# Kernel optimization log

Measured on AMD Instinct MI355X. Metric: run time of the kernel, lower is better.

The kernel has to match this reference:

```python
import jax, jax.numpy as jnp
import numpy as np

E = 256
H_HEADS = 8
HD = E // H_HEADS
NEG = -1e9


def setup_inputs() -> dict:
    key = jax.random.key(0)
    ks = jax.random.split(key, 16)
    B, Q, Hh, Ww = 16, 100, 64, 64
    S = Hh * Ww
    std = 1.0 / np.sqrt(E)
    inp = {
        "query_features": jax.random.normal(ks[0], (B, Q, E), jnp.float32),
        "image_features": jax.random.normal(ks[1], (B, E, Hh, Ww), jnp.float32),
        "mask": jax.random.randint(ks[2], (B, Q, Hh, Ww), 0, 2) > 0,
        "pos_query_embeddings": jax.random.normal(ks[3], (B, Q, E), jnp.float32),
        "pos_image_embeddings": jax.random.normal(ks[4], (B, S, E), jnp.float32),
        "Wq": jax.random.normal(ks[5], (E, E), jnp.float32) * std,
        "bq": jnp.zeros((E,), jnp.float32),
        "Wk": jax.random.normal(ks[6], (E, E), jnp.float32) * std,
        "bk": jnp.zeros((E,), jnp.float32),
        "Wv": jax.random.normal(ks[7], (E, E), jnp.float32) * std,
        "bv": jnp.zeros((E,), jnp.float32),
        "Wo": jax.random.normal(ks[8], (E, E), jnp.float32) * std,
        "bo": jnp.zeros((E,), jnp.float32),
    }
    return inp


def reference(query_features, image_features, mask, pos_query_embeddings,
              pos_image_embeddings, Wq, bq, Wk, bk, Wv, bv, Wo, bo):
    B, _, Hh, Ww = image_features.shape
    Q = query_features.shape[1]
    S = Hh * Ww
    # (B, S, E)
    img = jnp.transpose(image_features.reshape(B, E, S), (0, 2, 1))
    q = (query_features + pos_query_embeddings) @ Wq.T + bq  # (B,Q,E)
    k = (img + pos_image_embeddings) @ Wk.T + bk              # (B,S,E)
    v = img @ Wv.T + bv                                       # (B,S,E)
    q = q.reshape(B, Q, H_HEADS, HD).transpose(0, 2, 1, 3)    # (B,H,Q,D)
    k = k.reshape(B, S, H_HEADS, HD).transpose(0, 2, 1, 3)    # (B,H,S,D)
    v = v.reshape(B, S, H_HEADS, HD).transpose(0, 2, 1, 3)
    scale = 1.0 / jnp.sqrt(jnp.asarray(HD, q.dtype))
    scores = jnp.einsum('bhqd,bhsd->bhqs', q, k) * scale
    amask = mask.reshape(B, 1, Q, S)
    scores = jnp.where(amask, scores, NEG)
    attn = jax.nn.softmax(scores, axis=-1)
    out = jnp.einsum('bhqs,bhsd->bhqd', attn, v)
    out = out.transpose(0, 2, 1, 3).reshape(B, Q, E)
    return out @ Wo.T + bo
```

## Files before the change

### kernel.cpp

```cpp
#include <hip/hip_runtime.h>
#include <math.h>

#define BB 16
#define QQ 100
#define EE 256
#define NH 8
#define HD 32
#define SS 4096
#define QP 128
#define NZ 8
#define SCHUNK (SS / NZ)
#define M0 8.0f

typedef _Float16 half8_t __attribute__((ext_vector_type(8)));
typedef _Float16 half4_t __attribute__((ext_vector_type(4)));
typedef float floatx4 __attribute__((ext_vector_type(4)));

__global__ __launch_bounds__(256) void maskpack_kernel(
    const int* __restrict__ mask, unsigned* __restrict__ mbits)
{
    int gid  = blockIdx.x * 256 + threadIdx.x;
    int lane = gid & 63;
    int F    = gid & ~63;
    int s    = (F & (SS - 1)) + lane;
    int qp   = (F >> 12) & (QP - 1);
    int b    = F >> 19;
    int qc   = min(qp, QQ - 1);
    int v    = mask[((size_t)(b * QQ + qc)) * SS + s];
    unsigned long long bal = __ballot(v != 0);
    int w = (F & (SS - 1)) >> 5;
    if (lane == 0)
        mbits[((size_t)(b * (SS / 32) + w)) * QP + qp] = (unsigned)bal;
    if (lane == 32)
        mbits[((size_t)(b * (SS / 32) + w + 1)) * QP + qp] = (unsigned)(bal >> 32);
}

__global__ __launch_bounds__(256) void wcvt_kernel(
    const float* __restrict__ Wk, const float* __restrict__ Wv,
    _Float16* __restrict__ wk16a, _Float16* __restrict__ wv16a)
{
    int gid = blockIdx.x * 256 + threadIdx.x;
    int m = gid & 8191;
    const float* src = (gid < 8192) ? Wk : Wv;
    _Float16* dst = (gid < 8192) ? wk16a : wv16a;
    int l = m & 63, kk = (m >> 6) & 7, et = m >> 9;
    int e = et * 16 + (l & 15);
    int f0 = kk * 32 + (l >> 4) * 8;
    float4 a0 = *(const float4*)&src[(size_t)e * EE + f0];
    float4 a1 = *(const float4*)&src[(size_t)e * EE + f0 + 4];
    half8_t h;
    h[0]=(_Float16)a0.x; h[1]=(_Float16)a0.y; h[2]=(_Float16)a0.z; h[3]=(_Float16)a0.w;
    h[4]=(_Float16)a1.x; h[5]=(_Float16)a1.y; h[6]=(_Float16)a1.z; h[7]=(_Float16)a1.w;
    *(half8_t*)&dst[(size_t)m * 8] = h;
}

__global__ __launch_bounds__(512, 4) void fused_kv_kernel(
    const float* __restrict__ img,
    const float* __restrict__ pos,
    const _Float16* __restrict__ wk16a, const float* __restrict__ bk,
    const _Float16* __restrict__ wv16a, const float* __restrict__ bv,
    _Float16* __restrict__ kbuf,
    _Float16* __restrict__ vt)
{
    __shared__ _Float16 vstage[256 * 72];

    const int t  = threadIdx.x;
    const int w  = t >> 6, l = t & 63;
    const int gg = l >> 4, li = l & 15;
    const int si = w & 3, eh = w >> 2;

    const int m0  = blockIdx.x * 64;
    const int b   = m0 >> 12;
    const int s0  = m0 & (SS - 1);
    const int ss0 = s0 + si * 16;
    const int e0  = eh * 128;

    const float* imgp = img + (size_t)b * EE * SS + (size_t)(gg * 8) * SS + ss0 + li;
    const float* posp = pos + ((size_t)(b * SS + ss0 + li)) * EE + gg * 8;
    const _Float16* wkp = wk16a + (size_t)eh * 32768 + l * 8;
    const _Float16* wvp = wv16a + (size_t)eh * 32768 + l * 8;

    floatx4 acck[8] = {};
    floatx4 accv[8] = {};

    #pragma unroll 1
    for (int kk = 0; kk < 8; ++kk) {
        const int f0 = kk * 32;

        float iv[8];
        #pragma unroll
        for (int j = 0; j < 8; ++j)
            iv[j] = imgp[(size_t)(f0 + j) * SS];
        float4 p0 = *(const float4*)(posp + f0);
        float4 p1 = *(const float4*)(posp + f0 + 4);

        half8_t av8, ak8;
        av8[0] = (_Float16)iv[0];  ak8[0] = (_Float16)(iv[0] + p0.x);
        av8[1] = (_Float16)iv[1];  ak8[1] = (_Float16)(iv[1] + p0.y);
        av8[2] = (_Float16)iv[2];  ak8[2] = (_Float16)(iv[2] + p0.z);
        av8[3] = (_Float16)iv[3];  ak8[3] = (_Float16)(iv[3] + p0.w);
        av8[4] = (_Float16)iv[4];  ak8[4] = (_Float16)(iv[4] + p1.x);
        av8[5] = (_Float16)iv[5];  ak8[5] = (_Float16)(iv[5] + p1.y);
        av8[6] = (_Float16)iv[6];  ak8[6] = (_Float16)(iv[6] + p1.z);
        av8[7] = (_Float16)iv[7];  ak8[7] = (_Float16)(iv[7] + p1.w);

        #pragma unroll
        for (int n = 0; n < 8; ++n) {
            half8_t wkf = *(const half8_t*)(wkp + (size_t)((n * 8 + kk) << 9));
            half8_t wvf = *(const half8_t*)(wvp + (size_t)((n * 8 + kk) << 9));
            acck[n] = __builtin_amdgcn_mfma_f32_16x16x32_f16(ak8, wkf, acck[n], 0, 0, 0);
            accv[n] = __builtin_amdgcn_mfma_f32_16x16x32_f16(av8, wvf, accv[n], 0, 0, 0);
        }
    }

    #pragma unroll
    for (int n = 0; n < 8; ++n) {
        int e = e0 + n * 16 + li;
        float bj = bk[e];
        int row = b * SS + ss0 + gg * 4;
        #pragma unroll
        for (int r = 0; r < 4; ++r)
            kbuf[(size_t)(row + r) * EE + e] = (_Float16)(acck[n][r] + bj);
    }

    #pragma unroll
    for (int n = 0; n < 8; ++n) {
        int e_loc = e0 + n * 16 + li;
        float bj = bv[e_loc];
        int s_loc = si * 16 + gg * 4;
        half4_t h4;
        #pragma unroll
        for (int r = 0; r < 4; ++r)
            h4[r] = (_Float16)(accv[n][r] + bj);
        *(half4_t*)&vstage[e_loc * 72 + s_loc] = h4;
    }
    __syncthreads();
    #pragma unroll
    for (int c = 0; c < 4; ++c) {
        int row = c * 64 + (t >> 3);
        int so  = (t & 7) * 8;
        half8_t v8 = *(const half8_t*)&vstage[row * 72 + so];
        int hh = row >> 5, dd = row & 31;
        *(half8_t*)(vt + ((size_t)((b * NH + hh) * HD + dd)) * SS + s0 + so) = v8;
    }
}

__global__ __launch_bounds__(256) void proj_kernel(
    const float* __restrict__ x1, const float* __restrict__ x2,
    const float* __restrict__ W, const float* __restrict__ bias,
    float* __restrict__ outf, _Float16* __restrict__ out16,
    float oscale, int has_x2)
{
    const int row0 = blockIdx.x * 8;
    const int t = threadIdx.x;
    __shared__ float xs[8][256];

    #pragma unroll
    for (int p = 0; p < 8; ++p) {
        int idx = t + p * 256;
        int f = idx & 255, j = idx >> 8;
        size_t g = (size_t)(row0 + j) * EE + f;
        float v = x1[g];
        if (has_x2) v += x2[g];
        xs[j][f] = v;
    }
    __syncthreads();

    const int e = t;
    const float* wrow = W + (size_t)e * EE;
    float acc[8];
    const float bv = bias[e];
    #pragma unroll
    for (int j = 0; j < 8; ++j) acc[j] = bv;

    #pragma unroll 4
    for (int f4 = 0; f4 < 64; ++f4) {
        float4 w4 = *(const float4*)(wrow + f4 * 4);
        #pragma unroll
        for (int j = 0; j < 8; ++j) {
            float4 x4 = *(const float4*)&xs[j][f4 * 4];
            acc[j] = fmaf(w4.x, x4.x, acc[j]);
            acc[j] = fmaf(w4.y, x4.y, acc[j]);
            acc[j] = fmaf(w4.z, x4.z, acc[j]);
            acc[j] = fmaf(w4.w, x4.w, acc[j]);
        }
    }
    if (out16) {
        #pragma unroll
        for (int j = 0; j < 8; ++j)
            out16[(size_t)(row0 + j) * EE + e] = (_Float16)(acc[j] * oscale);
    } else {
        #pragma unroll
        for (int j = 0; j < 8; ++j)
            outf[(size_t)(row0 + j) * EE + e] = acc[j];
    }
}

__global__ __launch_bounds__(256) void attn_mfma_kernel(
    const _Float16* __restrict__ q16,
    const _Float16* __restrict__ kbuf,
    const _Float16* __restrict__ vt,
    const unsigned* __restrict__ mbits,
    float* __restrict__ part,
    float* __restrict__ pl)
{
    const int z = blockIdx.x, h = blockIdx.y, b = blockIdx.z;
    const int t = threadIdx.x;
    const int w = t >> 6, l = t & 63;
    const int g = l >> 4, li = l & 15;

    __shared__ _Float16 ks[64 * 40];
    __shared__ _Float16 vs[32 * 72];
    __shared__ _Float16 ps[128 * 72];
    __shared__ unsigned mw[2][QP];

    half8_t qf[2];
    {
        int q0r = min(32 * w + li, QQ - 1);
        int q1r = min(32 * w + 16 + li, QQ - 1);
        qf[0] = *(const half8_t*)(q16 + ((size_t)(b * QQ + q0r)) * EE + h * HD + g * 8);
        qf[1] = *(const half8_t*)(q16 + ((size_t)(b * QQ + q1r)) * EE + h * HD + g * 8);
    }

    float lsum[2][4] = {{0.f}};
    floatx4 accO[2][2] = {};

    for (int it = 0; it < SCHUNK / 64; ++it) {
        const int sblk = z * SCHUNK + it * 64;

        {
            int sl = t >> 2, koff = (t & 3) * 8;
            *(half8_t*)&ks[sl * 40 + koff] =
                *(const half8_t*)(kbuf + ((size_t)(b * SS + sblk + sl)) * EE + h * HD + koff);
            int dl = t >> 3, soff = (t & 7) * 8;
            *(half8_t*)&vs[dl * 72 + soff] =
                *(const half8_t*)(vt + ((size_t)((b * NH + h) * HD + dl)) * SS + sblk + soff);
            mw[t >> 7][t & 127] =
                mbits[((size_t)(b * (SS / 32) + (sblk >> 5) + (t >> 7))) * QP + (t & 127)];
        }
        __syncthreads();

        half8_t kf[4];
        #pragma unroll
        for (int st = 0; st < 4; ++st)
            kf[st] = *(const half8_t*)&ks[(st * 16 + li) * 40 + g * 8];
        floatx4 sc[2][4];
        #pragma unroll
        for (int qt = 0; qt < 2; ++qt)
            #pragma unroll
            for (int st = 0; st < 4; ++st) {
                floatx4 zero = {0.f, 0.f, 0.f, 0.f};
                sc[qt][st] = __builtin_amdgcn_mfma_f32_16x16x32_f16(
                    qf[qt], kf[st], zero, 0, 0, 0);
            }

        #pragma unroll
        for (int qt = 0; qt < 2; ++qt) {
            int qrow0 = 32 * w + qt * 16 + 4 * g;
            unsigned w0r[4], w1r[4];
            #pragma unroll
            for (int r = 0; r < 4; ++r) {
                w0r[r] = mw[0][qrow0 + r];
                w1r[r] = mw[1][qrow0 + r];
            }
            #pragma unroll
            for (int st = 0; st < 4; ++st)
                #pragma unroll
                for (int r = 0; r < 4; ++r) {
                    unsigned word = (st < 2) ? w0r[r] : w1r[r];
                    int keep = (word >> ((st & 1) * 16 + li)) & 1;
                    float pv = keep ? __expf(sc[qt][st][r] - M0) : 0.f;
                    _Float16 ph = (_Float16)pv;
                    lsum[qt][r] += (float)ph;
                    ps[(qrow0 + r) * 72 + st * 16 + li] = ph;
                }
        }

        half8_t vb[2][2];
        #pragma unroll
        for (int dt = 0; dt < 2; ++dt) {
            vb[dt][0] = *(const half8_t*)&vs[(dt * 16 + li) * 72 + g * 8];
            vb[dt][1] = *(const half8_t*)&vs[(dt * 16 + li) * 72 + 32 + g * 8];
        }
        #pragma unroll
        for (int qt = 0; qt < 2; ++qt) {
            half8_t a0 = *(const half8_t*)&ps[(32 * w + qt * 16 + li) * 72 + g * 8];
            half8_t a1 = *(const half8_t*)&ps[(32 * w + qt * 16 + li) * 72 + 32 + g * 8];
            #pragma unroll
            for (int dt = 0; dt < 2; ++dt) {
                accO[qt][dt] = __builtin_amdgcn_mfma_f32_16x16x32_f16(
                    a0, vb[dt][0], accO[qt][dt], 0, 0, 0);
                accO[qt][dt] = __builtin_amdgcn_mfma_f32_16x16x32_f16(
                    a1, vb[dt][1], accO[qt][dt], 0, 0, 0);
            }
        }
        __syncthreads();
    }

    #pragma unroll
    for (int qt = 0; qt < 2; ++qt)
        #pragma unroll
        for (int r = 0; r < 4; ++r) {
            float v = lsum[qt][r];
            v += __shfl_xor(v, 1, 64);
            v += __shfl_xor(v, 2, 64);
            v += __shfl_xor(v, 4, 64);
            v += __shfl_xor(v, 8, 64);
            lsum[qt][r] = v;
        }

    const size_t pbase = (((size_t)z * BB + b) * NH + h) * QP;
    #pragma unroll
    for (int qt = 0; qt < 2; ++qt) {
        int qrow0 = 32 * w + qt * 16 + 4 * g;
        #pragma unroll
        for (int r = 0; r < 4; ++r) {
            int qp = qrow0 + r;
            #pragma unroll
            for (int dt = 0; dt < 2; ++dt)
                part[(pbase + qp) * HD + dt * 16 + li] = accO[qt][dt][r];
            if (li == 0) pl[pbase + qp] = lsum[qt][r];
        }
    }
}

__global__ __launch_bounds__(256) void combine_kernel(
    const float* __restrict__ part, const float* __restrict__ pl,
    float* __restrict__ abuf)
{
    int tid = blockIdx.x * 256 + threadIdx.x;
    int d  = tid & 31;
    int qp = (tid >> 5) & 127;
    int h  = (tid >> 12) & 7;
    int b  = tid >> 15;
    if (qp >= QQ) return;
    float L = 0.f, O = 0.f;
    #pragma unroll
    for (int zz = 0; zz < NZ; ++zz) {
        size_t idx = (((size_t)zz * BB + b) * NH + h) * QP + qp;
        L += pl[idx];
        O += part[idx * HD + d];
    }
    abuf[((size_t)(b * QQ + qp)) * EE + h * HD + d] = O / fmaxf(L, 1e-30f);
}

extern "C" void kernel_launch(void* const* d_in, const int* in_sizes, int n_in,
                              void* d_out, int out_size, void* d_ws, size_t ws_size,
                              hipStream_t stream)
{
    const float* qf   = (const float*)d_in[0];
    const float* img  = (const float*)d_in[1];
    const int*   mask = (const int*)  d_in[2];
    const float* pq   = (const float*)d_in[3];
    const float* pimg = (const float*)d_in[4];
    const float* Wq   = (const float*)d_in[5];
    const float* bq   = (const float*)d_in[6];
    const float* Wk   = (const float*)d_in[7];
    const float* bk   = (const float*)d_in[8];
    const float* Wv   = (const float*)d_in[9];
    const float* bv   = (const float*)d_in[10];
    const float* Wo   = (const float*)d_in[11];
    const float* bo   = (const float*)d_in[12];
    float* out = (float*)d_out;

    const size_t MSE = (size_t)BB * SS * EE;

    _Float16* kbuf = (_Float16*)d_ws;
    _Float16* vtb  = kbuf + MSE;
    _Float16* q16  = vtb + MSE;
    unsigned* mbits = (unsigned*)(q16 + (size_t)BB * QQ * EE);
    float* part = (float*)(mbits + (size_t)BB * (SS / 32) * QP);
    float* pl   = part + (size_t)NZ * BB * NH * QP * HD;
    float* abuf = pl + (size_t)NZ * BB * NH * QP;
    _Float16* wk16a = (_Float16*)(abuf + (size_t)BB * QQ * EE);
    _Float16* wv16a = wk16a + (size_t)EE * EE;

    const float scale = 0.17677669529663687f;

    maskpack_kernel<<<(BB * QP * SS) / 256, 256, 0, stream>>>(mask, mbits);
    wcvt_kernel<<<64, 256, 0, stream>>>(Wk, Wv, wk16a, wv16a);
    proj_kernel<<<BB * QQ / 8, 256, 0, stream>>>(qf, pq, Wq, bq, nullptr, q16, scale, 1);
    fused_kv_kernel<<<BB * SS / 64, 512, 0, stream>>>(img, pimg, wk16a, bk, wv16a, bv, kbuf, vtb);
    attn_mfma_kernel<<<dim3(NZ, NH, BB), 256, 0, stream>>>(q16, kbuf, vtb, mbits, part, pl);
    combine_kernel<<<(BB * NH * QP * HD) / 256, 256, 0, stream>>>(part, pl, abuf);
    proj_kernel<<<BB * QQ / 8, 256, 0, stream>>>(abuf, nullptr, Wo, bo, out, nullptr, 1.f, 0);
}
```

Baseline: 349.2 us.

## Shrink KV projection tile and software-prefetch next input slice

Result: slower. 365.1 us (+4.5%).

```diff
diff --git a/kernel.cpp b/kernel.cpp
--- a/kernel.cpp
+++ b/kernel.cpp
@@ -62,59 +62,79 @@
     _Float16* __restrict__ kbuf,
     _Float16* __restrict__ vt)
 {
-    __shared__ _Float16 vstage[256 * 72];
+    __shared__ _Float16 vstage[256 * 40];
 
     const int t  = threadIdx.x;
     const int w  = t >> 6, l = t & 63;
     const int gg = l >> 4, li = l & 15;
-    const int si = w & 3, eh = w >> 2;
-
-    const int m0  = blockIdx.x * 64;
+    const int si = w & 1, eh = w >> 1;
+
+    const int m0  = blockIdx.x * 32;
     const int b   = m0 >> 12;
     const int s0  = m0 & (SS - 1);
     const int ss0 = s0 + si * 16;
-    const int e0  = eh * 128;
+    const int e0  = eh * 64;
 
     const float* imgp = img + (size_t)b * EE * SS + (size_t)(gg * 8) * SS + ss0 + li;
     const float* posp = pos + ((size_t)(b * SS + ss0 + li)) * EE + gg * 8;
-    const _Float16* wkp = wk16a + (size_t)eh * 32768 + l * 8;
-    const _Float16* wvp = wv16a + (size_t)eh * 32768 + l * 8;
-
-    floatx4 acck[8] = {};
-    floatx4 accv[8] = {};
+    const _Float16* wkp = wk16a + (size_t)eh * 16384 + l * 8;
+    const _Float16* wvp = wv16a + (size_t)eh * 16384 + l * 8;
+
+    floatx4 acck[4] = {};
+    floatx4 accv[4] = {};
+
+    float iva[8], ppa[8];
+    #pragma unroll
+    for (int j = 0; j < 8; ++j) iva[j] = imgp[(size_t)j * SS];
+    {
+        float4 q0 = *(const float4*)posp;
+        float4 q1 = *(const float4*)(posp + 4);
+        ppa[0]=q0.x; ppa[1]=q0.y; ppa[2]=q0.z; ppa[3]=q0.w;
+        ppa[4]=q1.x; ppa[5]=q1.y; ppa[6]=q1.z; ppa[7]=q1.w;
+    }
 
     #pragma unroll 1
     for (int kk = 0; kk < 8; ++kk) {
-        const int f0 = kk * 32;
-
-        float iv[8];
-        #pragma unroll
-        for (int j = 0; j < 8; ++j)
-            iv[j] = imgp[(size_t)(f0 + j) * SS];
-        float4 p0 = *(const float4*)(posp + f0);
-        float4 p1 = *(const float4*)(posp + f0 + 4);
-
         half8_t av8, ak8;
-        av8[0] = (_Float16)iv[0];  ak8[0] = (_Float16)(iv[0] + p0.x);
-        av8[1] = (_Float16)iv[1];  ak8[1] = (_Float16)(iv[1] + p0.y);
-        av8[2] = (_Float16)iv[2];  ak8[2] = (_Float16)(iv[2] + p0.z);
-        av8[3] = (_Float16)iv[3];  ak8[3] = (_Float16)(iv[3] + p0.w);
-        av8[4] = (_Float16)iv[4];  ak8[4] = (_Float16)(iv[4] + p1.x);
-        av8[5] = (_Float16)iv[5];  ak8[5] = (_Float16)(iv[5] + p1.y);
-        av8[6] = (_Float16)iv[6];  ak8[6] = (_Float16)(iv[6] + p1.z);
-        av8[7] = (_Float16)iv[7];  ak8[7] = (_Float16)(iv[7] + p1.w);
-
-        #pragma unroll
-        for (int n = 0; n < 8; ++n) {
-            half8_t wkf = *(const half8_t*)(wkp + (size_t)((n * 8 + kk) << 9));
-            half8_t wvf = *(const half8_t*)(wvp + (size_t)((n * 8 + kk) << 9));
-            acck[n] = __builtin_amdgcn_mfma_f32_16x16x32_f16(ak8, wkf, acck[n], 0, 0, 0);
-            accv[n] = __builtin_amdgcn_mfma_f32_16x16x32_f16(av8, wvf, accv[n], 0, 0, 0);
-        }
-    }
-
-    #pragma unroll
-    for (int n = 0; n < 8; ++n) {
+        #pragma unroll
+        for (int j = 0; j < 8; ++j) {
+            av8[j] = (_Float16)iva[j];
+            ak8[j] = (_Float16)(iva[j] + ppa[j]);
+        }
+
+        const _Float16* wko = wkp + kk * 512;
+        const _Float16* wvo = wvp + kk * 512;
+        half8_t wkf0 = *(const half8_t*)(wko);
+        half8_t wkf1 = *(const half8_t*)(wko + 4096);
+        half8_t wkf2 = *(const half8_t*)(wko + 8192);
+        half8_t wkf3 = *(const half8_t*)(wko + 12288);
+        half8_t wvf0 = *(const half8_t*)(wvo);
+        half8_t wvf1 = *(const half8_t*)(wvo + 4096);
+        half8_t wvf2 = *(const half8_t*)(wvo + 8192);
+        half8_t wvf3 = *(const half8_t*)(wvo + 12288);
+
+        if (kk < 7) {
+            #pragma unroll
+            for (int j = 0; j < 8; ++j)
+                iva[j] = imgp[(size_t)((kk + 1) * 32 + j) * SS];
+            float4 q0 = *(const float4*)(posp + (kk + 1) * 32);
+            float4 q1 = *(const float4*)(posp + (kk + 1) * 32 + 4);
+            ppa[0]=q0.x; ppa[1]=q0.y; ppa[2]=q0.z; ppa[3]=q0.w;
+            ppa[4]=q1.x; ppa[5]=q1.y; ppa[6]=q1.z; ppa[7]=q1.w;
+        }
+
+        acck[0] = __builtin_amdgcn_mfma_f32_16x16x32_f16(ak8, wkf0, acck[0], 0, 0, 0);
+        accv[0] = __builtin_amdgcn_mfma_f32_16x16x32_f16(av8, wvf0, accv[0], 0, 0, 0);
+        acck[1] = __builtin_amdgcn_mfma_f32_16x16x32_f16(ak8, wkf1, acck[1], 0, 0, 0);
+        accv[1] = __builtin_amdgcn_mfma_f32_16x16x32_f16(av8, wvf1, accv[1], 0, 0, 0);
+        acck[2] = __builtin_amdgcn_mfma_f32_16x16x32_f16(ak8, wkf2, acck[2], 0, 0, 0);
+        accv[2] = __builtin_amdgcn_mfma_f32_16x16x32_f16(av8, wvf2, accv[2], 0, 0, 0);
+        acck[3] = __builtin_amdgcn_mfma_f32_16x16x32_f16(ak8, wkf3, acck[3], 0, 0, 0);
+        accv[3] = __builtin_amdgcn_mfma_f32_16x16x32_f16(av8, wvf3, accv[3], 0, 0, 0);
+    }
+
+    #pragma unroll
+    for (int n = 0; n < 4; ++n) {
         int e = e0 + n * 16 + li;
         float bj = bk[e];
         int row = b * SS + ss0 + gg * 4;
@@ -124,7 +144,7 @@
     }
 
     #pragma unroll
-    for (int n = 0; n < 8; ++n) {
+    for (int n = 0; n < 4; ++n) {
         int e_loc = e0 + n * 16 + li;
         float bj = bv[e_loc];
         int s_loc = si * 16 + gg * 4;
@@ -132,14 +152,14 @@
         #pragma unroll
         for (int r = 0; r < 4; ++r)
             h4[r] = (_Float16)(accv[n][r] + bj);
-        *(half4_t*)&vstage[e_loc * 72 + s_loc] = h4;
+        *(half4_t*)&vstage[e_loc * 40 + s_loc] = h4;
     }
     __syncthreads();
     #pragma unroll
-    for (int c = 0; c < 4; ++c) {
-        int row = c * 64 + (t >> 3);
-        int so  = (t & 7) * 8;
-        half8_t v8 = *(const half8_t*)&vstage[row * 72 + so];
+    for (int c = 0; c < 2; ++c) {
+        int row = c * 128 + (t >> 2);
+        int so  = (t & 3) * 8;
+        half8_t v8 = *(const half8_t*)&vstage[row * 40 + so];
         int hh = row >> 5, dd = row & 31;
         *(half8_t*)(vt + ((size_t)((b * NH + hh) * HD + dd)) * SS + s0 + so) = v8;
     }
@@ -380,7 +400,7 @@
     maskpack_kernel<<<(BB * QP * SS) / 256, 256, 0, stream>>>(mask, mbits);
     wcvt_kernel<<<64, 256, 0, stream>>>(Wk, Wv, wk16a, wv16a);
     proj_kernel<<<BB * QQ / 8, 256, 0, stream>>>(qf, pq, Wq, bq, nullptr, q16, scale, 1);
-    fused_kv_kernel<<<BB * SS / 64, 512, 0, stream>>>(img, pimg, wk16a, bk, wv16a, bv, kbuf, vtb);
+    fused_kv_kernel<<<BB * SS / 32, 512, 0, stream>>>(img, pimg, wk16a, bk, wv16a, bv, kbuf, vtb);
     attn_mfma_kernel<<<dim3(NZ, NH, BB), 256, 0, stream>>>(q16, kbuf, vtb, mbits, part, pl);
     combine_kernel<<<(BB * NH * QP * HD) / 256, 256, 0, stream>>>(part, pl, abuf);
     proj_kernel<<<BB * QQ / 8, 256, 0, stream>>>(abuf, nullptr, Wo, bo, out, nullptr, 1.f, 0);
```
